# Performance work log

Measured on AMD Instinct MI355X. Metric: run time of the kernel, lower is better.

Reference implementation:

```python
import jax, jax.numpy as jnp
import numpy as np

B, N, D, C, K = 32, 4096, 768, 10, 16


def setup_inputs() -> dict:
    key = jax.random.key(0)
    k1, k2, k3, k4, k5 = jax.random.split(key, 5)
    H = jax.random.normal(k1, (B, N, D), dtype=jnp.float32)
    # nn.Linear default init scale ~ 1/sqrt(fan_in)
    sc = 1.0 / np.sqrt(D)
    w_score = jax.random.uniform(k2, (D,), jnp.float32, -sc, sc)
    b_score = jax.random.uniform(k3, (), jnp.float32, -sc, sc)
    W_cls = jax.random.uniform(k4, (D, C), jnp.float32, -sc, sc)
    b_cls = jax.random.uniform(k5, (C,), jnp.float32, -sc, sc)
    return {"H": H, "w_score": w_score, "b_score": b_score,
            "W_cls": W_cls, "b_cls": b_cls}


def reference(H, w_score, b_score, W_cls, b_cls):
    # scores per instance: [B, N]
    s = jnp.einsum("bnd,d->bn", H, w_score) + b_score
    k = min(K, H.shape[1])
    _, topk = jax.lax.top_k(s, k)                      # [B, k] int32
    # gather top-k instances: [B, k, D]
    Hk = jnp.take_along_axis(H, topk[:, :, None], axis=1)
    M = jnp.mean(Hk, axis=1)                           # [B, D]
    # dropout is identity in eval mode
    logits = M @ W_cls + b_cls                         # [B, C]
    # attention mask: scatter 1.0 at topk indices, normalize
    A = jnp.zeros_like(s).at[jnp.arange(H.shape[0])[:, None], topk].set(1.0)
    A = A / jnp.maximum(A.sum(axis=1, keepdims=True), 1e-6)
    return logits, A[:, :, None]
```

## Files before the change

kernel.cpp:

```cpp
#include <hip/hip_runtime.h>
#include <math.h>

#define BB 32
#define NN 4096
#define DD 768
#define CC 10
#define KK 16

__global__ __launch_bounds__(256) void score_kernel(
    const float* __restrict__ H, const float* __restrict__ w,
    const float* __restrict__ b_score, float* __restrict__ s) {
  __shared__ __align__(16) float ws[DD];
  for (int i = threadIdx.x; i < DD; i += 256) ws[i] = w[i];
  __syncthreads();

  const int wave = threadIdx.x >> 6;
  const int lane = threadIdx.x & 63;
  const long row = (long)blockIdx.x * 4 + wave;

  const float4* Hrow = (const float4*)(H + row * DD);
  const float4* wv4 = (const float4*)ws;

  float acc = 0.f;
#pragma unroll
  for (int j = 0; j < 3; ++j) {
    const int p = lane + j * 64;
    float4 h = Hrow[p];
    float4 wv = wv4[p];
    acc += h.x * wv.x + h.y * wv.y + h.z * wv.z + h.w * wv.w;
  }
#pragma unroll
  for (int off = 32; off >= 1; off >>= 1) acc += __shfl_xor(acc, off, 64);

  if (lane == 0) s[row] = acc + b_score[0];
}

__global__ __launch_bounds__(256) void tail_kernel(
    const float* __restrict__ s, const float* __restrict__ H,
    const float* __restrict__ Wc, const float* __restrict__ bc,
    float* __restrict__ logits, float* __restrict__ A) {
  const int b = blockIdx.x;
  const int t = threadIdx.x;
  const int wave = t >> 6;
  const int lane = t & 63;

  __shared__ float wv[4];
  __shared__ int wi[4];
  __shared__ int winners[KK];
  __shared__ float M[DD];
  __shared__ float wp[4][CC];

  float v[16];
  {
    const float4* sv4 = (const float4*)(s + (long)b * NN);
    float4 a0 = sv4[t * 4 + 0];
    float4 a1 = sv4[t * 4 + 1];
    float4 a2 = sv4[t * 4 + 2];
    float4 a3 = sv4[t * 4 + 3];
    v[0] = a0.x;  v[1] = a0.y;  v[2] = a0.z;  v[3] = a0.w;
    v[4] = a1.x;  v[5] = a1.y;  v[6] = a1.z;  v[7] = a1.w;
    v[8] = a2.x;  v[9] = a2.y;  v[10] = a2.z; v[11] = a2.w;
    v[12] = a3.x; v[13] = a3.y; v[14] = a3.z; v[15] = a3.w;
  }

  float lv = v[0];
  int li = t * 16;
#pragma unroll
  for (int j = 1; j < 16; ++j)
    if (v[j] > lv) { lv = v[j]; li = t * 16 + j; }

  for (int k = 0; k < KK; ++k) {
    float rv = lv;
    int ri = li;
#pragma unroll
    for (int off = 1; off < 64; off <<= 1) {
      float ov = __shfl_xor(rv, off, 64);
      int oi = __shfl_xor(ri, off, 64);
      if (ov > rv || (ov == rv && oi < ri)) { rv = ov; ri = oi; }
    }
    if (lane == 0) { wv[wave] = rv; wi[wave] = ri; }
    __syncthreads();

    float bv = wv[0];
    int bi = wi[0];
#pragma unroll
    for (int wq = 1; wq < 4; ++wq) {
      float ov = wv[wq];
      int oi = wi[wq];
      if (ov > bv || (ov == bv && oi < bi)) { bv = ov; bi = oi; }
    }
    if (t == 0) winners[k] = bi;

    if ((bi >> 4) == t) {
      const int slot = bi & 15;
#pragma unroll
      for (int j = 0; j < 16; ++j)
        if (j == slot) v[j] = -INFINITY;
      lv = -INFINITY;
      li = t * 16;
#pragma unroll
      for (int j = 0; j < 16; ++j)
        if (v[j] > lv) { lv = v[j]; li = t * 16 + j; }
    }
    __syncthreads();
  }

#pragma unroll
  for (int jj = 0; jj < 4; ++jj) {
    const int q = t + jj * 256;
    const int n0 = q * 4;
    float4 av = {0.f, 0.f, 0.f, 0.f};
#pragma unroll
    for (int k = 0; k < KK; ++k) {
      int d = winners[k] - n0;
      if (d == 0) av.x = 0.0625f;
      else if (d == 1) av.y = 0.0625f;
      else if (d == 2) av.z = 0.0625f;
      else if (d == 3) av.w = 0.0625f;
    }
    ((float4*)(A + (long)b * NN))[q] = av;
  }

  for (int d = t; d < DD; d += 256) {
    float acc = 0.f;
#pragma unroll
    for (int k = 0; k < KK; ++k)
      acc += H[((long)b * NN + winners[k]) * DD + d];
    M[d] = acc * (1.f / 16.f);
  }
  __syncthreads();

  float part[CC];
#pragma unroll
  for (int c = 0; c < CC; ++c) part[c] = 0.f;
  for (int d = t; d < DD; d += 256) {
    float m = M[d];
#pragma unroll
    for (int c = 0; c < CC; ++c) part[c] += m * Wc[d * CC + c];
  }
#pragma unroll
  for (int off = 32; off >= 1; off >>= 1) {
#pragma unroll
    for (int c = 0; c < CC; ++c) part[c] += __shfl_xor(part[c], off, 64);
  }
  if (lane == 0) {
#pragma unroll
    for (int c = 0; c < CC; ++c) wp[wave][c] = part[c];
  }
  __syncthreads();
  if (t < CC) {
    float r = wp[0][t] + wp[1][t] + wp[2][t] + wp[3][t];
    logits[b * CC + t] = r + bc[t];
  }
}

extern "C" void kernel_launch(void* const* d_in, const int* in_sizes, int n_in,
                              void* d_out, int out_size, void* d_ws, size_t ws_size,
                              hipStream_t stream) {
  const float* H = (const float*)d_in[0];
  const float* w_score = (const float*)d_in[1];
  const float* b_score = (const float*)d_in[2];
  const float* W_cls = (const float*)d_in[3];
  const float* b_cls = (const float*)d_in[4];

  float* out = (float*)d_out;
  float* logits = out;
  float* A = out + BB * CC;

  float* s = (float*)d_ws;

  score_kernel<<<BB * NN / 4, 256, 0, stream>>>(H, w_score, b_score, s);
  tail_kernel<<<BB, 256, 0, stream>>>(s, H, W_cls, b_cls, logits, A);
}
```

Before: 101.3 us.

## Process sixteen rows per wave in score kernel with register-held weights

The score kernel now launches 2048 blocks, and each wave computes 16 rows in four batches of four. The score weights are loaded into registers once per wave instead of being staged through shared memory. Each batch issues twelve float4 loads together to raise memory-level parallelism, and the four results are written as one float4. The tail kernel also drops the shared M buffer and its barrier by folding the top-k mean directly into the classifier accumulation. The main cost targeted is per-block launch and sync overhead on a bandwidth-bound H read, at the price of fewer waves in flight.

```diff
diff --git a/kernel.cpp b/kernel.cpp
--- a/kernel.cpp
+++ b/kernel.cpp
@@ -10,29 +10,53 @@
 __global__ __launch_bounds__(256) void score_kernel(
     const float* __restrict__ H, const float* __restrict__ w,
     const float* __restrict__ b_score, float* __restrict__ s) {
-  __shared__ __align__(16) float ws[DD];
-  for (int i = threadIdx.x; i < DD; i += 256) ws[i] = w[i];
-  __syncthreads();
+  const int wave_id = blockIdx.x * 4 + (threadIdx.x >> 6);
+  const int lane = threadIdx.x & 63;
 
-  const int wave = threadIdx.x >> 6;
-  const int lane = threadIdx.x & 63;
-  const long row = (long)blockIdx.x * 4 + wave;
+  const float4* __restrict__ w4 = (const float4*)w;
+  const float4 w0 = w4[lane];
+  const float4 w1 = w4[lane + 64];
+  const float4 w2 = w4[lane + 128];
+  const float bs = b_score[0];
 
-  const float4* Hrow = (const float4*)(H + row * DD);
-  const float4* wv4 = (const float4*)ws;
+  const long row0 = (long)wave_id * 16;
+  const float4* __restrict__ H4 = (const float4*)H;
 
-  float acc = 0.f;
+  for (int it = 0; it < 4; ++it) {
+    const long r = row0 + it * 4;
+    const float4* __restrict__ p = H4 + r * 192;
+
+    float4 h[4][3];
 #pragma unroll
-  for (int j = 0; j < 3; ++j) {
-    const int p = lane + j * 64;
-    float4 h = Hrow[p];
-    float4 wv = wv4[p];
-    acc += h.x * wv.x + h.y * wv.y + h.z * wv.z + h.w * wv.w;
+    for (int rr = 0; rr < 4; ++rr)
+#pragma unroll
+      for (int j = 0; j < 3; ++j)
+        h[rr][j] = p[rr * 192 + lane + j * 64];
+
+    float acc[4];
+#pragma unroll
+    for (int rr = 0; rr < 4; ++rr) {
+      float a = h[rr][0].x * w0.x + h[rr][0].y * w0.y +
+                h[rr][0].z * w0.z + h[rr][0].w * w0.w;
+      a += h[rr][1].x * w1.x + h[rr][1].y * w1.y +
+           h[rr][1].z * w1.z + h[rr][1].w * w1.w;
+      a += h[rr][2].x * w2.x + h[rr][2].y * w2.y +
+           h[rr][2].z * w2.z + h[rr][2].w * w2.w;
+      acc[rr] = a;
+    }
+
+#pragma unroll
+    for (int off = 32; off >= 1; off >>= 1) {
+#pragma unroll
+      for (int rr = 0; rr < 4; ++rr)
+        acc[rr] += __shfl_xor(acc[rr], off, 64);
+    }
+
+    if (lane == 0) {
+      float4 o = {acc[0] + bs, acc[1] + bs, acc[2] + bs, acc[3] + bs};
+      ((float4*)s)[r >> 2] = o;
+    }
   }
-#pragma unroll
-  for (int off = 32; off >= 1; off >>= 1) acc += __shfl_xor(acc, off, 64);
-
-  if (lane == 0) s[row] = acc + b_score[0];
 }
 
 __global__ __launch_bounds__(256) void tail_kernel(
@@ -47,7 +71,6 @@
   __shared__ float wv[4];
   __shared__ int wi[4];
   __shared__ int winners[KK];
-  __shared__ float M[DD];
   __shared__ float wp[4][CC];
 
   float v[16];
@@ -121,22 +144,17 @@
     ((float4*)(A + (long)b * NN))[q] = av;
   }
 
-  for (int d = t; d < DD; d += 256) {
-    float acc = 0.f;
-#pragma unroll
-    for (int k = 0; k < KK; ++k)
-      acc += H[((long)b * NN + winners[k]) * DD + d];
-    M[d] = acc * (1.f / 16.f);
-  }
-  __syncthreads();
-
   float part[CC];
 #pragma unroll
   for (int c = 0; c < CC; ++c) part[c] = 0.f;
   for (int d = t; d < DD; d += 256) {
-    float m = M[d];
+    float g = 0.f;
 #pragma unroll
-    for (int c = 0; c < CC; ++c) part[c] += m * Wc[d * CC + c];
+    for (int k = 0; k < KK; ++k)
+      g += H[((long)b * NN + winners[k]) * DD + d];
+    g *= (1.f / 16.f);
+#pragma unroll
+    for (int c = 0; c < CC; ++c) part[c] += g * Wc[d * CC + c];
   }
 #pragma unroll
   for (int off = 32; off >= 1; off >>= 1) {
@@ -169,6 +187,6 @@
 
   float* s = (float*)d_ws;
 
-  score_kernel<<<BB * NN / 4, 256, 0, stream>>>(H, w_score, b_score, s);
+  score_kernel<<<2048, 256, 0, stream>>>(H, w_score, b_score, s);
   tail_kernel<<<BB, 256, 0, stream>>>(s, H, W_cls, b_cls, logits, A);
 }
```

Measured after the change: 105.5 us. +4.1%, slower.
